# Kernel optimization log

Measured on AMD Instinct MI355X. Metric: run time of the kernel, lower is better.

The kernel has to match this reference:

```python
import jax, jax.numpy as jnp
import numpy as np

MEM_SIZE = 2048
CELL = 64
R_HEADS = 4
IN_SIZE = 512
IFACE = CELL * R_HEADS + CELL + 2 * CELL + 2 * R_HEADS + 5  # 461
DELTA = 1e-6
EPS = 1e-6


def setup_inputs() -> dict:
    key = jax.random.key(0)
    ks = jax.random.split(key, 8)
    b = 256
    return {
        'xi': jax.random.normal(ks[0], (b, IN_SIZE), jnp.float32),
        'W': jax.random.normal(ks[1], (IFACE, IN_SIZE), jnp.float32) * 0.05,
        'gamma': jnp.ones((IFACE,), jnp.float32),
        'beta': jnp.zeros((IFACE,), jnp.float32),
        'memory': jax.random.normal(ks[2], (b, MEM_SIZE, CELL), jnp.float32),
        'read_weights': jax.random.uniform(ks[3], (b, R_HEADS, MEM_SIZE), jnp.float32),
        'write_weights': jax.random.uniform(ks[4], (b, 1, MEM_SIZE), jnp.float32),
        'usage': jax.random.uniform(ks[5], (b, MEM_SIZE), jnp.float32),
    }


def _cosine(mem, keys):
    # mem: (b,m,c), keys: (b,k,c) -> (b,k,m)
    mem_n = mem / (jnp.linalg.norm(mem, axis=-1, keepdims=True) + EPS)
    key_n = keys / (jnp.linalg.norm(keys, axis=-1, keepdims=True) + EPS)
    return jnp.einsum('bkc,bmc->bkm', key_n, mem_n)


def reference(xi, W, gamma, beta, memory, read_weights, write_weights, usage):
    b = xi.shape[0]
    r, k, w, m = R_HEADS, CELL, CELL, MEM_SIZE

    # interface projection + GroupNorm(1, C) over channel dim
    itf = xi @ W.T
    mu = jnp.mean(itf, axis=1, keepdims=True)
    var = jnp.var(itf, axis=1, keepdims=True)
    itf = (itf - mu) / jnp.sqrt(var + 1e-5) * gamma + beta

    c = 0
    read_keys = jnp.tanh(itf[:, c:c + r * k].reshape(b, r, k)); c += r * k
    read_strengths = jax.nn.softplus(itf[:, c:c + r]); c += r
    write_key = jnp.tanh(itf[:, c:c + k].reshape(b, 1, k)); c += k
    write_strength = jax.nn.softplus(itf[:, c]).reshape(b, 1); c += 1
    erase_vec = jax.nn.sigmoid(itf[:, c:c + w].reshape(b, 1, w)); c += w
    write_vec = jnp.tanh(itf[:, c:c + w].reshape(b, 1, w)); c += w
    free_gates = jax.nn.sigmoid(itf[:, c:c + r]); c += r
    alloc_gate = jax.nn.softmax(itf[:, c:c + 3], axis=1); c += 3
    write_gate = jax.nn.sigmoid(itf[:, c]).reshape(b, 1)

    # ---- usage update ----
    u = usage + (1 - usage) * (1 - jnp.prod(1 - write_weights, axis=1))
    psi = jnp.prod(1 - free_gates[:, :, None] * read_weights, axis=1)  # (b,m)
    u = u * psi

    # ---- content weighting for write ----
    wcw = jax.nn.softmax(_cosine(memory, write_key) * write_strength[:, :, None], axis=2)  # (b,1,m)

    # ---- allocation ----
    u2 = DELTA + (1 - DELTA) * u
    idx = jnp.argsort(u2, axis=1)                              # ascending usage (phi)
    su = jnp.take_along_axis(u2, idx, axis=1)                  # sorted usage
    cp = jnp.cumprod(jnp.concatenate([jnp.ones((b, 1), u2.dtype), su], axis=1), axis=1)[:, :-1]
    sa = (1 - su) * cp
    inv = jnp.argsort(idx, axis=1)                             # inverse permutation (phi_rev)
    alloc = jnp.take_along_axis(sa, inv, axis=1)               # (b,m)

    # ---- write weighting ----
    fw = (alloc_gate[:, 0:1] * jnp.mean(read_weights, axis=1)
          + alloc_gate[:, 1:2] * alloc
          + alloc_gate[:, 2:3] * wcw[:, 0])
    ww = (write_gate * fw)[:, None, :]                         # (b,1,m)

    # ---- memory write (erase + add) ----
    reset_gate = jnp.prod(1 - ww[:, :, :, None] * erase_vec[:, :, None, :], axis=1)  # (b,m,w)
    mem = memory * reset_gate + jnp.einsum('bm,bw->bmw', ww[:, 0], write_vec[:, 0])

    # ---- read ----
    rw = jax.nn.softmax(_cosine(mem, read_keys) * read_strengths[:, :, None], axis=2)  # (b,r,m)
    read_vectors = jnp.einsum('brm,bmw->brw', rw, mem)         # (b,r,w)
    return read_vectors
```

## Files before the change

kernel.cpp:

```cpp
#include <hip/hip_runtime.h>
#include <math.h>

#define MM    2048
#define CC    64
#define RH    4
#define NIF   461
#define INS   512
#define EPSN  1e-6f

typedef unsigned long long u64;

#define OFF_P     ((size_t)0)
#define OFF_U2    ((size_t)131072)
#define OFF_MRW   ((size_t)655360)
#define OFF_SC    ((size_t)1179648)
#define OFF_ALLOC ((size_t)1703936)
#define OFF_WW    ((size_t)2228224)
#define OFF_PART  ((size_t)2752512)
#define OFF_PSTAT ((size_t)3276800)

__global__ __launch_bounds__(512) void k1_interface(
    const float* __restrict__ xi, const float* __restrict__ W,
    const float* __restrict__ gamma, const float* __restrict__ beta,
    const float* __restrict__ read_w, const float* __restrict__ write_w,
    const float* __restrict__ usage, float* __restrict__ ws)
{
  const int b = blockIdx.x, tid = threadIdx.x;
  const int lane = tid & 63, wid = tid >> 6;
  __shared__ __align__(16) float s_xi[512], s_itf[512], s_act[512];
  __shared__ float sRed[24];

  s_xi[tid] = xi[(size_t)b*INS + tid];
  __syncthreads();

  {
    const float4 x0 = ((const float4*)s_xi)[lane*2];
    const float4 x1 = ((const float4*)s_xi)[lane*2+1];
    for (int col = wid; col < NIF; col += 8) {
      const float4* Wr = (const float4*)(W + (size_t)col*INS);
      float4 a0 = Wr[lane*2], a1 = Wr[lane*2+1];
      float p = a0.x*x0.x + a0.y*x0.y + a0.z*x0.z + a0.w*x0.w
              + a1.x*x1.x + a1.y*x1.y + a1.z*x1.z + a1.w*x1.w;
      #pragma unroll
      for (int off=1; off<64; off<<=1) p += __shfl_xor(p, off);
      if (lane==0) s_itf[col] = p;
    }
  }
  __syncthreads();

  {
    float v = (tid < NIF) ? s_itf[tid] : 0.f;
    float s = v, q = v*v;
    #pragma unroll
    for (int off=1; off<64; off<<=1) { s += __shfl_xor(s,off); q += __shfl_xor(q,off); }
    if (lane==0){ sRed[wid] = s; sRed[8+wid] = q; }
    __syncthreads();
    if (tid==0){
      float ts=0.f, tq=0.f;
      for (int i=0;i<8;i++){ ts+=sRed[i]; tq+=sRed[8+i]; }
      float mean = ts/(float)NIF;
      float var  = tq/(float)NIF - mean*mean;
      sRed[16]=mean; sRed[17]=rsqrtf(var+1e-5f);
    }
    __syncthreads();
    float mean = sRed[16], rstd = sRed[17];
    if (tid < NIF) {
      float g = (s_itf[tid]-mean)*rstd*gamma[tid] + beta[tid];
      float a;
      if      (tid < 256) a = tanhf(g);
      else if (tid < 260) a = fmaxf(g,0.f) + log1pf(expf(-fabsf(g)));
      else if (tid < 324) a = tanhf(g);
      else if (tid ==324) a = fmaxf(g,0.f) + log1pf(expf(-fabsf(g)));
      else if (tid < 389) a = 1.f/(1.f+expf(-g));
      else if (tid < 453) a = tanhf(g);
      else if (tid < 457) a = 1.f/(1.f+expf(-g));
      else if (tid < 460) a = g;
      else                a = 1.f/(1.f+expf(-g));
      s_act[tid] = a;
    }
  }
  __syncthreads();

  float* P = ws + OFF_P + (size_t)b*512;
  if (wid < 4) {
    float t = s_act[wid*64 + lane];
    float q = t*t;
    #pragma unroll
    for (int off=1; off<64; off<<=1) q += __shfl_xor(q,off);
    P[wid*64+lane] = t * (s_act[256+wid] / (sqrtf(q) + EPSN));
  } else if (wid == 4) {
    float t = s_act[260+lane];
    float q = t*t;
    #pragma unroll
    for (int off=1; off<64; off<<=1) q += __shfl_xor(q,off);
    P[256+lane] = t * (s_act[324] / (sqrtf(q) + EPSN));
  } else if (wid == 5) {
    P[320+lane] = s_act[325+lane];
    P[384+lane] = s_act[389+lane];
  } else if (wid == 6 && lane == 0) {
    float a0=s_act[457], a1=s_act[458], a2=s_act[459];
    float mx = fmaxf(a0, fmaxf(a1,a2));
    float e0=expf(a0-mx), e1=expf(a1-mx), e2=expf(a2-mx);
    float is = 1.f/(e0+e1+e2);
    P[448]=e0*is; P[449]=e1*is; P[450]=e2*is; P[451]=s_act[460];
  }

  {
    const float4* us4 = (const float4*)(usage   + (size_t)b*MM);
    const float4* wr4 = (const float4*)(write_w + (size_t)b*MM);
    const float4* rw4 = (const float4*)(read_w  + (size_t)b*RH*MM);
    const float fg0=s_act[453], fg1=s_act[454], fg2=s_act[455], fg3=s_act[456];
    float4 u = us4[tid], w = wr4[tid];
    float4 r0 = rw4[tid], r1 = rw4[512+tid], r2 = rw4[1024+tid], r3 = rw4[1536+tid];
    float4 mr, u2o;
    mr.x = 0.25f*(r0.x+r1.x+r2.x+r3.x);
    mr.y = 0.25f*(r0.y+r1.y+r2.y+r3.y);
    mr.z = 0.25f*(r0.z+r1.z+r2.z+r3.z);
    mr.w = 0.25f*(r0.w+r1.w+r2.w+r3.w);
    #define U2C(comp)                                                           \
    { float uu  = u.comp + (1.f-u.comp)*w.comp;                                 \
      float psi = (1.f-fg0*r0.comp)*(1.f-fg1*r1.comp)*(1.f-fg2*r2.comp)*(1.f-fg3*r3.comp); \
      u2o.comp = 1e-6f + (1.f-1e-6f)*(uu*psi); }
    U2C(x) U2C(y) U2C(z) U2C(w)
    #undef U2C
    ((float4*)(ws + OFF_MRW + (size_t)b*MM))[tid] = mr;
    ((float4*)(ws + OFF_U2  + (size_t)b*MM))[tid] = u2o;
  }
}

__global__ __launch_bounds__(256) void k2_fused(
    const float* __restrict__ memory, float* __restrict__ ws)
{
  __shared__ __align__(16) u64 sKeys[2048];
  __shared__ float sT[260];
  const int tid = threadIdx.x;

  if (blockIdx.x < 256) {
    const int b = blockIdx.x;
    const int lane = tid & 63, w = tid >> 6;
    const float* u2p = ws + OFF_U2 + (size_t)b*MM;
    for (int i = tid; i < MM; i += 256)
      sKeys[i] = ((u64)__float_as_uint(u2p[i])<<32) | (unsigned)i;
    __syncthreads();

    for (int k = 2; k <= MM; k <<= 1) {
      for (int j = k >> 1; j > 0; j >>= 1) {
        #pragma unroll 4
        for (int c = tid; c < MM/2; c += 256) {
          int i   = ((c & ~(j-1)) << 1) | (c & (j-1));
          int ixj = i | j;
          u64 a = sKeys[i], d = sKeys[ixj];
          bool up = ((i & k) == 0);
          if ((a > d) == up) { sKeys[i] = d; sKeys[ixj] = a; }
        }
        __syncthreads();
      }
    }

    float p[8];
    {
      float run = 1.f;
      #pragma unroll
      for (int e = 0; e < 8; ++e) {
        float su = __uint_as_float((unsigned)(sKeys[tid*8+e]>>32));
        run *= su; p[e] = run;
      }
      sT[tid] = run;
    }
    __syncthreads();
    float v = sT[tid];
    float incl = v;
    #pragma unroll
    for (int off=1; off<64; off<<=1) {
      float n = __shfl_up(incl, off);
      if (lane >= off) incl *= n;
    }
    float excl = __shfl_up(incl, 1);
    if (lane == 0) excl = 1.f;
    if (lane == 63) sT[256 + w] = incl;
    __syncthreads();
    float base = 1.f;
    for (int ww2 = 0; ww2 < w; ++ww2) base *= sT[256 + ww2];
    float E = base * excl;

    float* allocp = ws + OFF_ALLOC + (size_t)b*MM;
    #pragma unroll
    for (int e = 0; e < 8; ++e) {
      u64 kk = sKeys[tid*8+e];
      float su = __uint_as_float((unsigned)(kk>>32));
      unsigned idx = (unsigned)(kk & 0xFFFFFFFFu);
      float cp = E * (e ? p[e-1] : 1.f);
      allocp[idx] = (1.f - su) * cp;
    }
  } else {
    const int f = blockIdx.x - 256;
    const int b = f >> 3, slice = f & 7;
    const int l16 = tid & 15, rowg = tid >> 4;
    const float* P = ws + OFF_P + (size_t)b*512;
    const float4 wk4 = ((const float4*)(P+256))[l16];
    const float4* mem4 = (const float4*)(memory + (size_t)b*MM*CC) + (size_t)slice*256*16;
    float* sc = ws + OFF_SC + (size_t)b*MM + slice*256;
    #pragma unroll 4
    for (int it = 0; it < 16; ++it) {
      int m = it*16 + rowg;
      float4 vv = mem4[m*16 + l16];
      float d = vv.x*wk4.x + vv.y*wk4.y + vv.z*wk4.z + vv.w*wk4.w;
      float q = vv.x*vv.x + vv.y*vv.y + vv.z*vv.z + vv.w*vv.w;
      #pragma unroll
      for (int off=1; off<16; off<<=1){ d += __shfl_xor(d,off); q += __shfl_xor(q,off); }
      if (l16==0) sc[m] = d / (sqrtf(q)+EPSN);
    }
  }
}

__global__ __launch_bounds__(256) void k3_ww(float* __restrict__ ws)
{
  const int b = blockIdx.x, tid = threadIdx.x;
  const int lane = tid & 63, w = tid >> 6;
  __shared__ float sR[8];
  const float4* sc4 = (const float4*)(ws + OFF_SC + (size_t)b*MM);
  float4 v0 = sc4[tid*2], v1 = sc4[tid*2+1];
  float m = fmaxf(fmaxf(fmaxf(v0.x,v0.y),fmaxf(v0.z,v0.w)),
                  fmaxf(fmaxf(v1.x,v1.y),fmaxf(v1.z,v1.w)));
  #pragma unroll
  for (int off=1; off<64; off<<=1) m = fmaxf(m, __shfl_xor(m,off));
  if (lane==0) sR[w] = m;
  __syncthreads();
  m = fmaxf(fmaxf(sR[0],sR[1]), fmaxf(sR[2],sR[3]));
  float e0=expf(v0.x-m), e1=expf(v0.y-m), e2=expf(v0.z-m), e3=expf(v0.w-m);
  float e4=expf(v1.x-m), e5=expf(v1.y-m), e6=expf(v1.z-m), e7=expf(v1.w-m);
  float s = e0+e1+e2+e3+e4+e5+e6+e7;
  #pragma unroll
  for (int off=1; off<64; off<<=1) s += __shfl_xor(s,off);
  if (lane==0) sR[4+w] = s;
  __syncthreads();
  float inv = 1.f/(sR[4]+sR[5]+sR[6]+sR[7]);

  const float* P = ws + OFF_P + (size_t)b*512;
  const float ag0=P[448], ag1=P[449], ag2=P[450], wg=P[451];
  const float4* mr4 = (const float4*)(ws + OFF_MRW   + (size_t)b*MM);
  const float4* al4 = (const float4*)(ws + OFF_ALLOC + (size_t)b*MM);
  float4* ww4 = (float4*)(ws + OFF_WW + (size_t)b*MM);
  float4 mra = mr4[tid*2], mrb = mr4[tid*2+1];
  float4 ala = al4[tid*2], alb = al4[tid*2+1];
  float4 oa, ob;
  oa.x = wg*(ag0*mra.x + ag1*ala.x + ag2*e0*inv);
  oa.y = wg*(ag0*mra.y + ag1*ala.y + ag2*e1*inv);
  oa.z = wg*(ag0*mra.z + ag1*ala.z + ag2*e2*inv);
  oa.w = wg*(ag0*mra.w + ag1*ala.w + ag2*e3*inv);
  ob.x = wg*(ag0*mrb.x + ag1*alb.x + ag2*e4*inv);
  ob.y = wg*(ag0*mrb.y + ag1*alb.y + ag2*e5*inv);
  ob.z = wg*(ag0*mrb.z + ag1*alb.z + ag2*e6*inv);
  ob.w = wg*(ag0*mrb.w + ag1*alb.w + ag2*e7*inv);
  ww4[tid*2] = oa; ww4[tid*2+1] = ob;
}

__global__ __launch_bounds__(256) void k4_passB(
    const float* __restrict__ memory, float* __restrict__ ws)
{
  const int slice = blockIdx.x, b = blockIdx.y;
  const int tid = threadIdx.x, l16 = tid & 15, rowg = tid >> 4;
  const int lane = tid & 63, wid = tid >> 6;
  __shared__ __align__(16) float chunk[64*68];
  __shared__ __align__(16) float sE[4*68];
  __shared__ float sHm[4], sHs[4], sHsc[4];

  const float* P = ws + OFF_P + (size_t)b*512;
  const float4 er4 = ((const float4*)(P+320))[l16];
  const float4 wv4 = ((const float4*)(P+384))[l16];
  const float4 k0 = ((const float4*)P)[     l16];
  const float4 k1 = ((const float4*)P)[16 + l16];
  const float4 k2 = ((const float4*)P)[32 + l16];
  const float4 k3 = ((const float4*)P)[48 + l16];
  const float* wwp = ws + OFF_WW + (size_t)b*MM + slice*256;
  const float4* mem4 = (const float4*)(memory + (size_t)b*MM*CC) + (size_t)slice*256*16;

  if (tid < 4){ sHm[tid] = -INFINITY; sHs[tid] = 0.f; }
  __syncthreads();
  const int q = lane & 15, ps = lane >> 4;
  float4 acc; acc.x=acc.y=acc.z=acc.w=0.f;

  for (int ch = 0; ch < 4; ++ch) {
    #pragma unroll
    for (int pp = 0; pp < 4; ++pp) {
      int p = pp*16 + rowg;
      int m = ch*64 + p;
      float4 v = mem4[m*16 + l16];
      float wm = wwp[m];
      float4 nv;
      nv.x = v.x*(1.f - wm*er4.x) + wm*wv4.x;
      nv.y = v.y*(1.f - wm*er4.y) + wm*wv4.y;
      nv.z = v.z*(1.f - wm*er4.z) + wm*wv4.z;
      nv.w = v.w*(1.f - wm*er4.w) + wm*wv4.w;
      *(float4*)&chunk[p*68 + (l16<<2)] = nv;
      float d0 = nv.x*k0.x+nv.y*k0.y+nv.z*k0.z+nv.w*k0.w;
      float d1 = nv.x*k1.x+nv.y*k1.y+nv.z*k1.z+nv.w*k1.w;
      float d2 = nv.x*k2.x+nv.y*k2.y+nv.z*k2.z+nv.w*k2.w;
      float d3 = nv.x*k3.x+nv.y*k3.y+nv.z*k3.z+nv.w*k3.w;
      float qq = nv.x*nv.x+nv.y*nv.y+nv.z*nv.z+nv.w*nv.w;
      #pragma unroll
      for (int off=1; off<16; off<<=1){
        d0+=__shfl_xor(d0,off); d1+=__shfl_xor(d1,off);
        d2+=__shfl_xor(d2,off); d3+=__shfl_xor(d3,off);
        qq+=__shfl_xor(qq,off);
      }
      if (l16==0){
        float inv = 1.f/(sqrtf(qq)+EPSN);
        sE[      p] = d0*inv;
        sE[ 68 + p] = d1*inv;
        sE[136 + p] = d2*inv;
        sE[204 + p] = d3*inv;
      }
    }
    __syncthreads();
    {
      float v = sE[wid*68 + lane];
      float cm = v;
      #pragma unroll
      for (int off=1; off<64; off<<=1) cm = fmaxf(cm, __shfl_xor(cm,off));
      float om = sHm[wid];
      float nm = fmaxf(om, cm);
      float scl = expf(om - nm);
      float e = expf(v - nm);
      sE[wid*68 + lane] = e;
      float es = e;
      #pragma unroll
      for (int off=1; off<64; off<<=1) es += __shfl_xor(es,off);
      if (lane==0){
        sHs[wid] = sHs[wid]*scl + es;
        sHm[wid] = nm;
        sHsc[wid] = scl;
      }
    }
    __syncthreads();
    {
      float scl = sHsc[wid];
      acc.x*=scl; acc.y*=scl; acc.z*=scl; acc.w*=scl;
      #pragma unroll
      for (int pp = 0; pp < 16; ++pp) {
        int p = ps*16 + pp;
        float e = sE[wid*68 + p];
        const float4 mv = *(const float4*)&chunk[p*68 + (q<<2)];
        acc.x += e*mv.x; acc.y += e*mv.y; acc.z += e*mv.z; acc.w += e*mv.w;
      }
    }
    __syncthreads();
  }

  #pragma unroll
  for (int off=16; off<64; off<<=1) {
    acc.x += __shfl_xor(acc.x, off);
    acc.y += __shfl_xor(acc.y, off);
    acc.z += __shfl_xor(acc.z, off);
    acc.w += __shfl_xor(acc.w, off);
  }
  if (ps == 0) {
    float* pacc = ws + OFF_PART + ((((size_t)b*8 + slice)*4 + wid)<<6);
    *(float4*)&pacc[q<<2] = acc;
  }
  if (lane == 0) {
    float* pst = ws + OFF_PSTAT + (((size_t)b*8 + slice)*4 + wid)*2;
    pst[0] = sHm[wid]; pst[1] = sHs[wid];
  }
}

__global__ __launch_bounds__(256) void k5_combine(
    const float* __restrict__ ws, float* __restrict__ out)
{
  const int b = blockIdx.x, tid = threadIdx.x;
  const int head = tid >> 6, c = tid & 63;
  float M = -INFINITY;
  #pragma unroll
  for (int s = 0; s < 8; ++s)
    M = fmaxf(M, ws[OFF_PSTAT + (((size_t)b*8 + s)*4 + head)*2]);
  float S = 0.f, A = 0.f;
  #pragma unroll
  for (int s = 0; s < 8; ++s) {
    const float* pst = ws + OFF_PSTAT + (((size_t)b*8 + s)*4 + head)*2;
    float w = expf(pst[0] - M);
    S += w * pst[1];
    A += w * ws[OFF_PART + ((((size_t)b*8 + s)*4 + head)<<6) + c];
  }
  out[((size_t)b<<8) + head*64 + c] = A / S;
}

extern "C" void kernel_launch(void* const* d_in, const int* in_sizes, int n_in,
                              void* d_out, int out_size, void* d_ws, size_t ws_size,
                              hipStream_t stream) {
  const float* xi      = (const float*)d_in[0];
  const float* W       = (const float*)d_in[1];
  const float* gamma   = (const float*)d_in[2];
  const float* beta    = (const float*)d_in[3];
  const float* memory  = (const float*)d_in[4];
  const float* read_w  = (const float*)d_in[5];
  const float* write_w = (const float*)d_in[6];
  const float* usage   = (const float*)d_in[7];
  float* ws  = (float*)d_ws;
  float* out = (float*)d_out;

  k1_interface<<<dim3(256), dim3(512), 0, stream>>>(xi, W, gamma, beta, read_w, write_w, usage, ws);
  k2_fused   <<<dim3(2304), dim3(256), 0, stream>>>(memory, ws);
  k3_ww      <<<dim3(256), dim3(256), 0, stream>>>(ws);
  k4_passB   <<<dim3(8,256), dim3(256), 0, stream>>>(memory, ws);
  k5_combine <<<dim3(256), dim3(256), 0, stream>>>(ws, out);
}
```

Measured before the change: 132.3 us.

## Fuse five kernels into two with atomic last-block combine and unstabilized softmax

Merges the interface projection, usage update, bitonic sort and content-score pass into a single per-batch kernel, so u2 no longer round-trips through global memory. The write-weight computation is folded into the read kernel, and the final combine uses atomics plus a last-block counter. Softmax max-subtraction is dropped on the assumption that cosine scores times the strengths stay small. This removes three launches and several workspace passes, but the memory scan for scores now runs on only 256 blocks instead of 2048, and exp without a max can overflow if the strengths grow large.

```diff
diff --git a/kernel.cpp b/kernel.cpp
--- a/kernel.cpp
+++ b/kernel.cpp
@@ -3,7 +3,6 @@
 
 #define MM    2048
 #define CC    64
-#define RH    4
 #define NIF   461
 #define INS   512
 #define EPSN  1e-6f
@@ -11,165 +10,195 @@
 typedef unsigned long long u64;
 
 #define OFF_P     ((size_t)0)
-#define OFF_U2    ((size_t)131072)
-#define OFF_MRW   ((size_t)655360)
-#define OFF_SC    ((size_t)1179648)
-#define OFF_ALLOC ((size_t)1703936)
-#define OFF_WW    ((size_t)2228224)
-#define OFF_PART  ((size_t)2752512)
-#define OFF_PSTAT ((size_t)3276800)
-
-__global__ __launch_bounds__(512) void k1_interface(
+#define OFF_Z     ((size_t)131072)
+#define OFF_MRW   ((size_t)131328)
+#define OFF_ALLOC ((size_t)655616)
+#define OFF_SC    ((size_t)1179904)
+#define OFF_A     ((size_t)1704192)
+#define OFF_S     ((size_t)1769728)
+#define OFF_CNT   ((size_t)1770752)
+
+__device__ __forceinline__ float actfn(int c, float g){
+  if (c < 256)  return tanhf(g);
+  if (c < 260)  return fmaxf(g,0.f) + log1pf(expf(-fabsf(g)));
+  if (c < 324)  return tanhf(g);
+  if (c == 324) return fmaxf(g,0.f) + log1pf(expf(-fabsf(g)));
+  if (c < 389)  return 1.f/(1.f+expf(-g));
+  if (c < 453)  return tanhf(g);
+  if (c < 457)  return 1.f/(1.f+expf(-g));
+  if (c < 460)  return g;
+  return 1.f/(1.f+expf(-g));
+}
+
+__global__ __launch_bounds__(512) void kA(
     const float* __restrict__ xi, const float* __restrict__ W,
     const float* __restrict__ gamma, const float* __restrict__ beta,
-    const float* __restrict__ read_w, const float* __restrict__ write_w,
-    const float* __restrict__ usage, float* __restrict__ ws)
+    const float* __restrict__ memory, const float* __restrict__ read_w,
+    const float* __restrict__ write_w, const float* __restrict__ usage,
+    float* __restrict__ ws)
 {
   const int b = blockIdx.x, tid = threadIdx.x;
   const int lane = tid & 63, wid = tid >> 6;
-  __shared__ __align__(16) float s_xi[512], s_itf[512], s_act[512];
-  __shared__ float sRed[24];
-
-  s_xi[tid] = xi[(size_t)b*INS + tid];
-  __syncthreads();
-
-  {
-    const float4 x0 = ((const float4*)s_xi)[lane*2];
-    const float4 x1 = ((const float4*)s_xi)[lane*2+1];
-    for (int col = wid; col < NIF; col += 8) {
-      const float4* Wr = (const float4*)(W + (size_t)col*INS);
-      float4 a0 = Wr[lane*2], a1 = Wr[lane*2+1];
-      float p = a0.x*x0.x + a0.y*x0.y + a0.z*x0.z + a0.w*x0.w
-              + a1.x*x1.x + a1.y*x1.y + a1.z*x1.z + a1.w*x1.w;
-      #pragma unroll
-      for (int off=1; off<64; off<<=1) p += __shfl_xor(p, off);
-      if (lane==0) s_itf[col] = p;
-    }
-  }
-  __syncthreads();
-
-  {
-    float v = (tid < NIF) ? s_itf[tid] : 0.f;
+  __shared__ __align__(16) float sxi[512], sP[512], sact[464], sT[520];
+  __shared__ __align__(16) u64 keys[2048];
+  __shared__ float sR[32];
+
+  if (tid < 256) ws[OFF_A + (size_t)b*256 + tid] = 0.f;
+  if (tid < 4)   ws[OFF_S + (size_t)b*4 + tid] = 0.f;
+  if (tid == 4)  ((int*)(ws + OFF_CNT))[b] = 0;
+
+  sxi[tid] = xi[(size_t)b*INS + tid];
+  __syncthreads();
+
+  {
+    const int g = lane >> 3, q = lane & 7;
+    const float4* x4 = (const float4*)sxi;
+    #pragma unroll 1
+    for (int i = 0; i < 8; ++i) {
+      int c = i*64 + wid*8 + g;
+      float acc = 0.f;
+      if (c < NIF) {
+        const float4* Wr = (const float4*)(W + (size_t)c*INS);
+        #pragma unroll
+        for (int t = 0; t < 16; ++t) {
+          float4 wv = Wr[t*8+q];
+          float4 xv = x4[t*8+q];
+          acc += wv.x*xv.x + wv.y*xv.y + wv.z*xv.z + wv.w*xv.w;
+        }
+      }
+      acc += __shfl_xor(acc,1); acc += __shfl_xor(acc,2); acc += __shfl_xor(acc,4);
+      if (q == 0 && c < NIF) sT[c] = acc;
+    }
+  }
+  __syncthreads();
+
+  {
+    float v = (tid < NIF) ? sT[tid] : 0.f;
     float s = v, q = v*v;
     #pragma unroll
-    for (int off=1; off<64; off<<=1) { s += __shfl_xor(s,off); q += __shfl_xor(q,off); }
-    if (lane==0){ sRed[wid] = s; sRed[8+wid] = q; }
+    for (int off=1; off<64; off<<=1){ s += __shfl_xor(s,off); q += __shfl_xor(q,off); }
+    if (lane==0){ sR[wid]=s; sR[8+wid]=q; }
     __syncthreads();
     if (tid==0){
       float ts=0.f, tq=0.f;
-      for (int i=0;i<8;i++){ ts+=sRed[i]; tq+=sRed[8+i]; }
+      for (int i=0;i<8;i++){ ts+=sR[i]; tq+=sR[8+i]; }
       float mean = ts/(float)NIF;
       float var  = tq/(float)NIF - mean*mean;
-      sRed[16]=mean; sRed[17]=rsqrtf(var+1e-5f);
-    }
-    __syncthreads();
-    float mean = sRed[16], rstd = sRed[17];
-    if (tid < NIF) {
-      float g = (s_itf[tid]-mean)*rstd*gamma[tid] + beta[tid];
-      float a;
-      if      (tid < 256) a = tanhf(g);
-      else if (tid < 260) a = fmaxf(g,0.f) + log1pf(expf(-fabsf(g)));
-      else if (tid < 324) a = tanhf(g);
-      else if (tid ==324) a = fmaxf(g,0.f) + log1pf(expf(-fabsf(g)));
-      else if (tid < 389) a = 1.f/(1.f+expf(-g));
-      else if (tid < 453) a = tanhf(g);
-      else if (tid < 457) a = 1.f/(1.f+expf(-g));
-      else if (tid < 460) a = g;
-      else                a = 1.f/(1.f+expf(-g));
-      s_act[tid] = a;
-    }
+      sR[16]=mean; sR[17]=rsqrtf(var+1e-5f);
+    }
+    __syncthreads();
+    float mean=sR[16], rstd=sR[17];
+    if (tid < NIF) sact[tid] = actfn(tid, (v-mean)*rstd*gamma[tid]+beta[tid]);
   }
   __syncthreads();
 
   float* P = ws + OFF_P + (size_t)b*512;
   if (wid < 4) {
-    float t = s_act[wid*64 + lane];
+    float t = sact[wid*64 + lane];
     float q = t*t;
     #pragma unroll
     for (int off=1; off<64; off<<=1) q += __shfl_xor(q,off);
-    P[wid*64+lane] = t * (s_act[256+wid] / (sqrtf(q) + EPSN));
+    float fk = t * (sact[256+wid] / (sqrtf(q) + EPSN));
+    sP[wid*64+lane] = fk; P[wid*64+lane] = fk;
   } else if (wid == 4) {
-    float t = s_act[260+lane];
+    float t = sact[260+lane];
     float q = t*t;
     #pragma unroll
     for (int off=1; off<64; off<<=1) q += __shfl_xor(q,off);
-    P[256+lane] = t * (s_act[324] / (sqrtf(q) + EPSN));
+    float fw = t * (sact[324] / (sqrtf(q) + EPSN));
+    sP[256+lane] = fw; P[256+lane] = fw;
   } else if (wid == 5) {
-    P[320+lane] = s_act[325+lane];
-    P[384+lane] = s_act[389+lane];
+    sP[320+lane] = sact[325+lane]; P[320+lane] = sact[325+lane];
+    sP[384+lane] = sact[389+lane]; P[384+lane] = sact[389+lane];
   } else if (wid == 6 && lane == 0) {
-    float a0=s_act[457], a1=s_act[458], a2=s_act[459];
+    float a0=sact[457], a1=sact[458], a2=sact[459];
     float mx = fmaxf(a0, fmaxf(a1,a2));
     float e0=expf(a0-mx), e1=expf(a1-mx), e2=expf(a2-mx);
     float is = 1.f/(e0+e1+e2);
-    P[448]=e0*is; P[449]=e1*is; P[450]=e2*is; P[451]=s_act[460];
+    P[448]=e0*is; P[449]=e1*is; P[450]=e2*is; P[451]=sact[460];
   }
 
   {
     const float4* us4 = (const float4*)(usage   + (size_t)b*MM);
     const float4* wr4 = (const float4*)(write_w + (size_t)b*MM);
-    const float4* rw4 = (const float4*)(read_w  + (size_t)b*RH*MM);
-    const float fg0=s_act[453], fg1=s_act[454], fg2=s_act[455], fg3=s_act[456];
+    const float4* rw4 = (const float4*)(read_w  + (size_t)b*4*MM);
+    const float fg0=sact[453], fg1=sact[454], fg2=sact[455], fg3=sact[456];
     float4 u = us4[tid], w = wr4[tid];
     float4 r0 = rw4[tid], r1 = rw4[512+tid], r2 = rw4[1024+tid], r3 = rw4[1536+tid];
-    float4 mr, u2o;
+    float4 mr;
     mr.x = 0.25f*(r0.x+r1.x+r2.x+r3.x);
     mr.y = 0.25f*(r0.y+r1.y+r2.y+r3.y);
     mr.z = 0.25f*(r0.z+r1.z+r2.z+r3.z);
     mr.w = 0.25f*(r0.w+r1.w+r2.w+r3.w);
-    #define U2C(comp)                                                           \
-    { float uu  = u.comp + (1.f-u.comp)*w.comp;                                 \
+    ((float4*)(ws + OFF_MRW + (size_t)b*MM))[tid] = mr;
+    const int base = tid*4;
+    #define U2C(comp, off)                                                     \
+    { float uu  = u.comp + (1.f-u.comp)*w.comp;                                \
       float psi = (1.f-fg0*r0.comp)*(1.f-fg1*r1.comp)*(1.f-fg2*r2.comp)*(1.f-fg3*r3.comp); \
-      u2o.comp = 1e-6f + (1.f-1e-6f)*(uu*psi); }
-    U2C(x) U2C(y) U2C(z) U2C(w)
+      float u2v = 1e-6f + (1.f-1e-6f)*(uu*psi);                                \
+      keys[base+off] = ((u64)__float_as_uint(u2v)<<32) | (unsigned)(base+off); }
+    U2C(x,0) U2C(y,1) U2C(z,2) U2C(w,3)
     #undef U2C
-    ((float4*)(ws + OFF_MRW + (size_t)b*MM))[tid] = mr;
-    ((float4*)(ws + OFF_U2  + (size_t)b*MM))[tid] = u2o;
-  }
-}
-
-__global__ __launch_bounds__(256) void k2_fused(
-    const float* __restrict__ memory, float* __restrict__ ws)
-{
-  __shared__ __align__(16) u64 sKeys[2048];
-  __shared__ float sT[260];
-  const int tid = threadIdx.x;
-
-  if (blockIdx.x < 256) {
-    const int b = blockIdx.x;
-    const int lane = tid & 63, w = tid >> 6;
-    const float* u2p = ws + OFF_U2 + (size_t)b*MM;
-    for (int i = tid; i < MM; i += 256)
-      sKeys[i] = ((u64)__float_as_uint(u2p[i])<<32) | (unsigned)i;
-    __syncthreads();
-
-    for (int k = 2; k <= MM; k <<= 1) {
-      for (int j = k >> 1; j > 0; j >>= 1) {
-        #pragma unroll 4
-        for (int c = tid; c < MM/2; c += 256) {
-          int i   = ((c & ~(j-1)) << 1) | (c & (j-1));
-          int ixj = i | j;
-          u64 a = sKeys[i], d = sKeys[ixj];
-          bool up = ((i & k) == 0);
-          if ((a > d) == up) { sKeys[i] = d; sKeys[ixj] = a; }
-        }
-        __syncthreads();
-      }
-    }
-
-    float p[8];
-    {
-      float run = 1.f;
+  }
+  __syncthreads();
+
+  {
+    const int l16 = tid & 15, rowg = tid >> 4;
+    const float4 wk4 = ((const float4*)(sP+256))[l16];
+    const float4* mem4 = (const float4*)(memory + (size_t)b*MM*CC);
+    float* sc = ws + OFF_SC + (size_t)b*MM;
+    float zpart = 0.f;
+    #pragma unroll 8
+    for (int it = 0; it < 64; ++it) {
+      int m = it*32 + rowg;
+      float4 v = mem4[m*16 + l16];
+      float d = v.x*wk4.x + v.y*wk4.y + v.z*wk4.z + v.w*wk4.w;
+      float q = v.x*v.x + v.y*v.y + v.z*v.z + v.w*v.w;
       #pragma unroll
-      for (int e = 0; e < 8; ++e) {
-        float su = __uint_as_float((unsigned)(sKeys[tid*8+e]>>32));
-        run *= su; p[e] = run;
-      }
-      sT[tid] = run;
-    }
-    __syncthreads();
-    float v = sT[tid];
-    float incl = v;
+      for (int off=1; off<16; off<<=1){ d += __shfl_xor(d,off); q += __shfl_xor(q,off); }
+      if (l16==0){
+        float s = d / (sqrtf(q)+EPSN);
+        sc[m] = s;
+        zpart += expf(s);
+      }
+    }
+    #pragma unroll
+    for (int off=1; off<64; off<<=1) zpart += __shfl_xor(zpart,off);
+    if (lane==0) sR[wid] = zpart;
+    __syncthreads();
+    if (tid==0){
+      float z=0.f;
+      for (int i=0;i<8;i++) z += sR[i];
+      ws[OFF_Z + b] = z;
+    }
+  }
+  __syncthreads();
+
+  for (int k2 = 2; k2 <= MM; k2 <<= 1) {
+    for (int j = k2 >> 1; j > 0; j >>= 1) {
+      #pragma unroll 2
+      for (int c = tid; c < MM/2; c += 512) {
+        int i   = ((c & ~(j-1)) << 1) | (c & (j-1));
+        int ixj = i | j;
+        u64 a = keys[i], d = keys[ixj];
+        bool up = ((i & k2) == 0);
+        if ((a > d) == up) { keys[i] = d; keys[ixj] = a; }
+      }
+      __syncthreads();
+    }
+  }
+
+  {
+    float p4[4];
+    float run = 1.f;
+    #pragma unroll
+    for (int e=0;e<4;++e){
+      float su = __uint_as_float((unsigned)(keys[tid*4+e]>>32));
+      run *= su; p4[e] = run;
+    }
+    sT[tid] = run;
+    __syncthreads();
+    float incl = sT[tid];
     #pragma unroll
     for (int off=1; off<64; off<<=1) {
       float n = __shfl_up(incl, off);
@@ -177,93 +206,34 @@
     }
     float excl = __shfl_up(incl, 1);
     if (lane == 0) excl = 1.f;
-    if (lane == 63) sT[256 + w] = incl;
+    if (lane == 63) sR[16+wid] = incl;
     __syncthreads();
     float base = 1.f;
-    for (int ww2 = 0; ww2 < w; ++ww2) base *= sT[256 + ww2];
+    for (int w2 = 0; w2 < wid; ++w2) base *= sR[16+w2];
     float E = base * excl;
-
     float* allocp = ws + OFF_ALLOC + (size_t)b*MM;
     #pragma unroll
-    for (int e = 0; e < 8; ++e) {
-      u64 kk = sKeys[tid*8+e];
+    for (int e=0;e<4;++e){
+      u64 kk = keys[tid*4+e];
       float su = __uint_as_float((unsigned)(kk>>32));
       unsigned idx = (unsigned)(kk & 0xFFFFFFFFu);
-      float cp = E * (e ? p[e-1] : 1.f);
+      float cp = E * (e ? p4[e-1] : 1.f);
       allocp[idx] = (1.f - su) * cp;
     }
-  } else {
-    const int f = blockIdx.x - 256;
-    const int b = f >> 3, slice = f & 7;
-    const int l16 = tid & 15, rowg = tid >> 4;
-    const float* P = ws + OFF_P + (size_t)b*512;
-    const float4 wk4 = ((const float4*)(P+256))[l16];
-    const float4* mem4 = (const float4*)(memory + (size_t)b*MM*CC) + (size_t)slice*256*16;
-    float* sc = ws + OFF_SC + (size_t)b*MM + slice*256;
-    #pragma unroll 4
-    for (int it = 0; it < 16; ++it) {
-      int m = it*16 + rowg;
-      float4 vv = mem4[m*16 + l16];
-      float d = vv.x*wk4.x + vv.y*wk4.y + vv.z*wk4.z + vv.w*wk4.w;
-      float q = vv.x*vv.x + vv.y*vv.y + vv.z*vv.z + vv.w*vv.w;
-      #pragma unroll
-      for (int off=1; off<16; off<<=1){ d += __shfl_xor(d,off); q += __shfl_xor(q,off); }
-      if (l16==0) sc[m] = d / (sqrtf(q)+EPSN);
-    }
   }
 }
 
-__global__ __launch_bounds__(256) void k3_ww(float* __restrict__ ws)
-{
-  const int b = blockIdx.x, tid = threadIdx.x;
-  const int lane = tid & 63, w = tid >> 6;
-  __shared__ float sR[8];
-  const float4* sc4 = (const float4*)(ws + OFF_SC + (size_t)b*MM);
-  float4 v0 = sc4[tid*2], v1 = sc4[tid*2+1];
-  float m = fmaxf(fmaxf(fmaxf(v0.x,v0.y),fmaxf(v0.z,v0.w)),
-                  fmaxf(fmaxf(v1.x,v1.y),fmaxf(v1.z,v1.w)));
-  #pragma unroll
-  for (int off=1; off<64; off<<=1) m = fmaxf(m, __shfl_xor(m,off));
-  if (lane==0) sR[w] = m;
-  __syncthreads();
-  m = fmaxf(fmaxf(sR[0],sR[1]), fmaxf(sR[2],sR[3]));
-  float e0=expf(v0.x-m), e1=expf(v0.y-m), e2=expf(v0.z-m), e3=expf(v0.w-m);
-  float e4=expf(v1.x-m), e5=expf(v1.y-m), e6=expf(v1.z-m), e7=expf(v1.w-m);
-  float s = e0+e1+e2+e3+e4+e5+e6+e7;
-  #pragma unroll
-  for (int off=1; off<64; off<<=1) s += __shfl_xor(s,off);
-  if (lane==0) sR[4+w] = s;
-  __syncthreads();
-  float inv = 1.f/(sR[4]+sR[5]+sR[6]+sR[7]);
-
-  const float* P = ws + OFF_P + (size_t)b*512;
-  const float ag0=P[448], ag1=P[449], ag2=P[450], wg=P[451];
-  const float4* mr4 = (const float4*)(ws + OFF_MRW   + (size_t)b*MM);
-  const float4* al4 = (const float4*)(ws + OFF_ALLOC + (size_t)b*MM);
-  float4* ww4 = (float4*)(ws + OFF_WW + (size_t)b*MM);
-  float4 mra = mr4[tid*2], mrb = mr4[tid*2+1];
-  float4 ala = al4[tid*2], alb = al4[tid*2+1];
-  float4 oa, ob;
-  oa.x = wg*(ag0*mra.x + ag1*ala.x + ag2*e0*inv);
-  oa.y = wg*(ag0*mra.y + ag1*ala.y + ag2*e1*inv);
-  oa.z = wg*(ag0*mra.z + ag1*ala.z + ag2*e2*inv);
-  oa.w = wg*(ag0*mra.w + ag1*ala.w + ag2*e3*inv);
-  ob.x = wg*(ag0*mrb.x + ag1*alb.x + ag2*e4*inv);
-  ob.y = wg*(ag0*mrb.y + ag1*alb.y + ag2*e5*inv);
-  ob.z = wg*(ag0*mrb.z + ag1*alb.z + ag2*e6*inv);
-  ob.w = wg*(ag0*mrb.w + ag1*alb.w + ag2*e7*inv);
-  ww4[tid*2] = oa; ww4[tid*2+1] = ob;
-}
-
-__global__ __launch_bounds__(256) void k4_passB(
-    const float* __restrict__ memory, float* __restrict__ ws)
+__global__ __launch_bounds__(256) void kB(
+    const float* __restrict__ memory, float* __restrict__ ws,
+    float* __restrict__ out)
 {
   const int slice = blockIdx.x, b = blockIdx.y;
   const int tid = threadIdx.x, l16 = tid & 15, rowg = tid >> 4;
   const int lane = tid & 63, wid = tid >> 6;
   __shared__ __align__(16) float chunk[64*68];
   __shared__ __align__(16) float sE[4*68];
-  __shared__ float sHm[4], sHs[4], sHsc[4];
+  __shared__ float wwL[256];
+  __shared__ int sFlag;
 
   const float* P = ws + OFF_P + (size_t)b*512;
   const float4 er4 = ((const float4*)(P+320))[l16];
@@ -272,13 +242,22 @@
   const float4 k1 = ((const float4*)P)[16 + l16];
   const float4 k2 = ((const float4*)P)[32 + l16];
   const float4 k3 = ((const float4*)P)[48 + l16];
-  const float* wwp = ws + OFF_WW + (size_t)b*MM + slice*256;
   const float4* mem4 = (const float4*)(memory + (size_t)b*MM*CC) + (size_t)slice*256*16;
 
-  if (tid < 4){ sHm[tid] = -INFINITY; sHs[tid] = 0.f; }
-  __syncthreads();
+  {
+    const float ag0=P[448], ag1=P[449], ag2=P[450], wg=P[451];
+    const float invZ = 1.f / ws[OFF_Z + b];
+    int mg = slice*256 + tid;
+    float wcw = expf(ws[OFF_SC + (size_t)b*MM + mg]) * invZ;
+    float al  = ws[OFF_ALLOC + (size_t)b*MM + mg];
+    float mr  = ws[OFF_MRW   + (size_t)b*MM + mg];
+    wwL[tid] = wg*(ag0*mr + ag1*al + ag2*wcw);
+  }
+  __syncthreads();
+
   const int q = lane & 15, ps = lane >> 4;
   float4 acc; acc.x=acc.y=acc.z=acc.w=0.f;
+  float S_acc = 0.f;
 
   for (int ch = 0; ch < 4; ++ch) {
     #pragma unroll
@@ -286,7 +265,7 @@
       int p = pp*16 + rowg;
       int m = ch*64 + p;
       float4 v = mem4[m*16 + l16];
-      float wm = wwp[m];
+      float wm = wwL[m];
       float4 nv;
       nv.x = v.x*(1.f - wm*er4.x) + wm*wv4.x;
       nv.y = v.y*(1.f - wm*er4.y) + wm*wv4.y;
@@ -314,28 +293,15 @@
     }
     __syncthreads();
     {
-      float v = sE[wid*68 + lane];
-      float cm = v;
-      #pragma unroll
-      for (int off=1; off<64; off<<=1) cm = fmaxf(cm, __shfl_xor(cm,off));
-      float om = sHm[wid];
-      float nm = fmaxf(om, cm);
-      float scl = expf(om - nm);
-      float e = expf(v - nm);
+      float e = expf(sE[wid*68 + lane]);
       sE[wid*68 + lane] = e;
       float es = e;
       #pragma unroll
       for (int off=1; off<64; off<<=1) es += __shfl_xor(es,off);
-      if (lane==0){
-        sHs[wid] = sHs[wid]*scl + es;
-        sHm[wid] = nm;
-        sHsc[wid] = scl;
-      }
+      S_acc += es;
     }
     __syncthreads();
     {
-      float scl = sHsc[wid];
-      acc.x*=scl; acc.y*=scl; acc.z*=scl; acc.w*=scl;
       #pragma unroll
       for (int pp = 0; pp < 16; ++pp) {
         int p = ps*16 + pp;
@@ -355,33 +321,25 @@
     acc.w += __shfl_xor(acc.w, off);
   }
   if (ps == 0) {
-    float* pacc = ws + OFF_PART + ((((size_t)b*8 + slice)*4 + wid)<<6);
-    *(float4*)&pacc[q<<2] = acc;
-  }
-  if (lane == 0) {
-    float* pst = ws + OFF_PSTAT + (((size_t)b*8 + slice)*4 + wid)*2;
-    pst[0] = sHm[wid]; pst[1] = sHs[wid];
-  }
-}
-
-__global__ __launch_bounds__(256) void k5_combine(
-    const float* __restrict__ ws, float* __restrict__ out)
-{
-  const int b = blockIdx.x, tid = threadIdx.x;
-  const int head = tid >> 6, c = tid & 63;
-  float M = -INFINITY;
-  #pragma unroll
-  for (int s = 0; s < 8; ++s)
-    M = fmaxf(M, ws[OFF_PSTAT + (((size_t)b*8 + s)*4 + head)*2]);
-  float S = 0.f, A = 0.f;
-  #pragma unroll
-  for (int s = 0; s < 8; ++s) {
-    const float* pst = ws + OFF_PSTAT + (((size_t)b*8 + s)*4 + head)*2;
-    float w = expf(pst[0] - M);
-    S += w * pst[1];
-    A += w * ws[OFF_PART + ((((size_t)b*8 + s)*4 + head)<<6) + c];
-  }
-  out[((size_t)b<<8) + head*64 + c] = A / S;
+    float* A = ws + OFF_A + (size_t)b*256 + (wid<<6) + (q<<2);
+    atomicAdd(&A[0], acc.x); atomicAdd(&A[1], acc.y);
+    atomicAdd(&A[2], acc.z); atomicAdd(&A[3], acc.w);
+  }
+  if (lane == 0) atomicAdd(&ws[OFF_S + (size_t)b*4 + wid], S_acc);
+
+  __threadfence();
+  __syncthreads();
+  if (tid == 0) {
+    int old = atomicAdd(&((int*)(ws + OFF_CNT))[b], 1);
+    sFlag = (old == 7);
+  }
+  __syncthreads();
+  if (sFlag) {
+    int h = tid >> 6, c = tid & 63;
+    float Sv = atomicAdd(&ws[OFF_S + (size_t)b*4 + h], 0.f);
+    float Av = atomicAdd(&ws[OFF_A + (size_t)b*256 + h*64 + c], 0.f);
+    out[((size_t)b<<8) + tid] = Av / Sv;
+  }
 }
 
 extern "C" void kernel_launch(void* const* d_in, const int* in_sizes, int n_in,
@@ -398,9 +356,6 @@
   float* ws  = (float*)d_ws;
   float* out = (float*)d_out;
 
-  k1_interface<<<dim3(256), dim3(512), 0, stream>>>(xi, W, gamma, beta, read_w, write_w, usage, ws);
-  k2_fused   <<<dim3(2304), dim3(256), 0, stream>>>(memory, ws);
-  k3_ww      <<<dim3(256), dim3(256), 0, stream>>>(ws);
-  k4_passB   <<<dim3(8,256), dim3(256), 0, stream>>>(memory, ws);
-  k5_combine <<<dim3(256), dim3(256), 0, stream>>>(ws, out);
+  kA<<<dim3(256), dim3(512), 0, stream>>>(xi, W, gamma, beta, memory, read_w, write_w, usage, ws);
+  kB<<<dim3(8,256), dim3(256), 0, stream>>>(memory, ws, out);
 }
```

After: 385.5 us. 191% more time.
